# Kernel tuning notes

Hardware: AMD Instinct MI355X
Metric: run time of the kernel (lower is better)

## Reference

```python
import jax, jax.numpy as jnp
import numpy as np

PAD_VALUE = -1e10  # matches torch F.pad(value=-1e10); padded cells are sliced away before output


def setup_inputs() -> dict:
    key = jax.random.key(0)
    x = jax.random.normal(key, (8, 16, 256, 256), dtype=jnp.float32)
    return {"x": x, "d": 5}


def reference(x, d):
    # x: (B, C, H, W). Builds a shift-graph: each pixel connects to the d*d-1
    # pixels in a d x d window; weight = -||f1-f2||^2 * sqrt(di^2+dj^2).
    B, C, H, W = x.shape
    r = d // 2
    id0 = jnp.arange(H * W, dtype=jnp.int32).reshape(H, W)
    img_pad = jnp.pad(x, ((0, 0), (0, 0), (r, r), (r, r)), constant_values=PAD_VALUE)
    ws, edges = [], []
    for i in range(d):
        for j in range(d):
            if i == r and j == r:
                continue
            pos_v = (i - r) * W + (j - r)
            # shifted view of the padded image, aligned with x: (B, C, H, W)
            f1 = img_pad[:, :, i:H + i, j:W + j]
            scale = float(((i - r) ** 2 + (j - r) ** 2) ** 0.5)
            dist = -((f1 - x) ** 2).sum(axis=1) * scale  # (B, H, W)
            # crop to the region where the shifted neighbor is in-bounds
            h0, h1 = max(r - i, 0), H - max(i - r, 0)
            w0, w1 = max(r - j, 0), W - max(j - r, 0)
            imgx = dist[:, h0:h1, w0:w1].reshape(B, -1)  # (B, n_ij)
            idx = id0[h0:h1, w0:w1].reshape(-1)          # (n_ij,)
            pos = jnp.broadcast_to(idx[None, :], (B, idx.shape[0]))
            ws.append(imgx)
            edges.append(jnp.stack((pos, pos + pos_v), axis=-1))  # (B, n_ij, 2)
    return jnp.concatenate(edges, axis=-2), jnp.concatenate(ws, axis=-1)
```

## Files before the change

### kernel.cpp

```cpp
#include <hip/hip_runtime.h>


#define HH 256
#define WW 256
#define CC 16
#define BB 8
#define HW (HH * WW)
#define EE 1557540

__global__ __launch_bounds__(256) void shiftgraph_kernel(
    const float* __restrict__ x, float* __restrict__ out) {
    __shared__ float lds[3080];
    const int bid = blockIdx.x;
    const int b = bid & 7;
    const int h = bid >> 3;
    const int w = threadIdx.x;

    const float* __restrict__ xb = x + (size_t)b * (CC * HW);

    const float* src[3];
    int dst[3];
#pragma unroll
    for (int inst = 0; inst < 3; ++inst) {
        const int flatf = inst * 1024 + w * 4;
        const int cl  = flatf / 768;
        const int rem = flatf - cl * 768;
        const int row = rem >> 8;
        const int col = rem & 255;
        int hr = h + row; hr = hr > HH - 1 ? HH - 1 : hr;
        src[inst] = xb + cl * HW + hr * WW + col;
        dst[inst] = flatf;
    }

    float* __restrict__ edges = out;
    float* __restrict__ wsp   = out + (size_t)BB * EE * 2;
    const size_t bE = (size_t)b * EE;
    const int posc = h * WW + w;

    float acc[12];
#pragma unroll
    for (int s2 = 0; s2 < 12; ++s2) acc[s2] = 0.0f;

#pragma unroll
    for (int cc = 0; cc < 4; ++cc) {
        if (cc > 0) {
            asm volatile("" ::: "memory");
            __builtin_amdgcn_s_barrier();
            __builtin_amdgcn_sched_barrier(0);
        }
#pragma unroll
        for (int inst = 0; inst < 3; ++inst) {
            const float4 v = *reinterpret_cast<const float4*>(src[inst]);
            *reinterpret_cast<float4*>(&lds[dst[inst]]) = v;
            src[inst] += 4 * HW;
        }
        asm volatile("s_waitcnt lgkmcnt(0)" ::: "memory");
        __builtin_amdgcn_s_barrier();
        __builtin_amdgcn_sched_barrier(0);

#pragma unroll
        for (int c = 0; c < 4; ++c) {
            const int base = c * 768 + w;
            const float ctr = lds[base];
            float d;
            d = lds[base + 1] - ctr; acc[0] = fmaf(d, d, acc[0]);
            d = lds[base + 2] - ctr; acc[1] = fmaf(d, d, acc[1]);
#pragma unroll
            for (int dj = -2; dj <= 2; ++dj) {
                d = lds[base + 256 + dj] - ctr;
                acc[4 + dj] = fmaf(d, d, acc[4 + dj]);
                d = lds[base + 512 + dj] - ctr;
                acc[9 + dj] = fmaf(d, d, acc[9 + dj]);
            }
        }

        {
            int s = 0;
#pragma unroll
            for (int di = 0; di <= 2; ++di) {
#pragma unroll
                for (int dj = (di == 0 ? 1 : -2); dj <= 2; ++dj, ++s) {
                    if (s < cc * 3 || s >= cc * 3 + 3) continue;
                    const int i = di + 2, j = dj + 2;
                    if (h + di >= HH) continue;
                    const int w2 = w + dj;
                    if (w2 < 0 || w2 >= WW) continue;

                    int offF = 0, offM = 0;
#pragma unroll
                    for (int m = 0; m < 25; ++m) {
                        const int mi = m / 5, mj = m % 5;
                        if (mi == 2 && mj == 2) continue;
                        const int cm = (HH - (mi < 2 ? 2 - mi : mi - 2)) *
                                       (WW - (mj < 2 ? 2 - mj : mj - 2));
                        if (m < i * 5 + j) offF += cm;
                        if (m < (4 - i) * 5 + (4 - j)) offM += cm;
                    }
                    const int cww = WW - (dj < 0 ? -dj : dj);
                    const int e1 = offF + h * cww + (w - (dj < 0 ? -dj : 0));
                    const int e2 = offM + h * cww + (w + (dj < 0 ? dj : 0));
                    const int posv = di * WW + dj;

                    *reinterpret_cast<float2*>(edges + (bE + e1) * 2) =
                        make_float2((float)posc, (float)(posc + posv));
                    *reinterpret_cast<float2*>(edges + (bE + e2) * 2) =
                        make_float2((float)(posc + posv), (float)posc);
                }
            }
        }
    }

    int s = 0;
#pragma unroll
    for (int di = 0; di <= 2; ++di) {
#pragma unroll
        for (int dj = (di == 0 ? 1 : -2); dj <= 2; ++dj, ++s) {
            const int i = di + 2, j = dj + 2;
            if (h + di >= HH) continue;
            const int w2 = w + dj;
            if (w2 < 0 || w2 >= WW) continue;

            const float scale = sqrtf((float)(di * di + dj * dj));
            const float wsv = -acc[s] * scale;

            int offF = 0, offM = 0;
#pragma unroll
            for (int m = 0; m < 25; ++m) {
                const int mi = m / 5, mj = m % 5;
                if (mi == 2 && mj == 2) continue;
                const int cm = (HH - (mi < 2 ? 2 - mi : mi - 2)) *
                               (WW - (mj < 2 ? 2 - mj : mj - 2));
                if (m < i * 5 + j) offF += cm;
                if (m < (4 - i) * 5 + (4 - j)) offM += cm;
            }
            const int cww = WW - (dj < 0 ? -dj : dj);
            const int e1 = offF + h * cww + (w - (dj < 0 ? -dj : 0));
            const int e2 = offM + h * cww + (w + (dj < 0 ? dj : 0));

            wsp[bE + e1] = wsv;
            wsp[bE + e2] = wsv;
        }
    }
}

extern "C" void kernel_launch(void* const* d_in, const int* in_sizes, int n_in,
                              void* d_out, int out_size, void* d_ws, size_t ws_size,
                              hipStream_t stream) {
    const float* x = (const float*)d_in[0];
    float* out = (float*)d_out;
    dim3 block(WW);
    dim3 grid(HH * BB);
    shiftgraph_kernel<<<grid, block, 0, stream>>>(x, out);
}
```

Before: 32.91 us.

## Transpose LDS tile to channel-interleaved float4 layout for vectorized neighbor reads

Each chunk of 4 channels is now staged in LDS as [row][col][channel], so one float4 LDS read returns all four channels of a neighbour pixel. This replaces 48 scalar LDS reads per chunk with 13 float4 reads. Global loads become 12 scalar loads per thread instead of 3 float4 loads, which costs some global load efficiency. Out-of-range columns are clamped rather than read past the row end.

```diff
diff --git a/kernel.cpp b/kernel.cpp
--- a/kernel.cpp
+++ b/kernel.cpp
@@ -10,7 +10,7 @@
 
 __global__ __launch_bounds__(256) void shiftgraph_kernel(
     const float* __restrict__ x, float* __restrict__ out) {
-    __shared__ float lds[3080];
+    __shared__ float lds[3072];
     const int bid = blockIdx.x;
     const int b = bid & 7;
     const int h = bid >> 3;
@@ -18,19 +18,19 @@
 
     const float* __restrict__ xb = x + (size_t)b * (CC * HW);
 
-    const float* src[3];
-    int dst[3];
+    const int ch = w & 3;
+    const int cq = w >> 2;
+    const float* prow[3];
 #pragma unroll
-    for (int inst = 0; inst < 3; ++inst) {
-        const int flatf = inst * 1024 + w * 4;
-        const int cl  = flatf / 768;
-        const int rem = flatf - cl * 768;
-        const int row = rem >> 8;
-        const int col = rem & 255;
-        int hr = h + row; hr = hr > HH - 1 ? HH - 1 : hr;
-        src[inst] = xb + cl * HW + hr * WW + col;
-        dst[inst] = flatf;
+    for (int r = 0; r < 3; ++r) {
+        int hr = h + r; hr = hr > HH - 1 ? HH - 1 : hr;
+        prow[r] = xb + ch * HW + hr * WW + cq;
     }
+
+    const int wp1 = w + 1 > 255 ? 255 : w + 1;
+    const int wp2 = w + 2 > 255 ? 255 : w + 2;
+    const int wm1 = w - 1 < 0 ? 0 : w - 1;
+    const int wm2 = w - 2 < 0 ? 0 : w - 2;
 
     float* __restrict__ edges = out;
     float* __restrict__ wsp   = out + (size_t)BB * EE * 2;
@@ -41,6 +41,8 @@
 #pragma unroll
     for (int s2 = 0; s2 < 12; ++s2) acc[s2] = 0.0f;
 
+    const float4* __restrict__ ldsv = reinterpret_cast<const float4*>(lds);
+
 #pragma unroll
     for (int cc = 0; cc < 4; ++cc) {
         if (cc > 0) {
@@ -49,29 +51,38 @@
             __builtin_amdgcn_sched_barrier(0);
         }
 #pragma unroll
-        for (int inst = 0; inst < 3; ++inst) {
-            const float4 v = *reinterpret_cast<const float4*>(src[inst]);
-            *reinterpret_cast<float4*>(&lds[dst[inst]]) = v;
-            src[inst] += 4 * HW;
+        for (int inst = 0; inst < 12; ++inst) {
+            const int r = inst >> 2, k = inst & 3;
+            lds[r * 1024 + k * 256 + w] = prow[r][(size_t)cc * 4 * HW + k * 64];
         }
         asm volatile("s_waitcnt lgkmcnt(0)" ::: "memory");
         __builtin_amdgcn_s_barrier();
         __builtin_amdgcn_sched_barrier(0);
 
-#pragma unroll
-        for (int c = 0; c < 4; ++c) {
-            const int base = c * 768 + w;
-            const float ctr = lds[base];
-            float d;
-            d = lds[base + 1] - ctr; acc[0] = fmaf(d, d, acc[0]);
-            d = lds[base + 2] - ctr; acc[1] = fmaf(d, d, acc[1]);
-#pragma unroll
-            for (int dj = -2; dj <= 2; ++dj) {
-                d = lds[base + 256 + dj] - ctr;
-                acc[4 + dj] = fmaf(d, d, acc[4 + dj]);
-                d = lds[base + 512 + dj] - ctr;
-                acc[9 + dj] = fmaf(d, d, acc[9 + dj]);
-            }
+        {
+            const float4 ctr = ldsv[w];
+            float4 nb; float dx, dy, dz, dw_;
+#define ACCUM(IDX, SLOT)                                                   \
+            nb = ldsv[IDX];                                                \
+            dx = nb.x - ctr.x; dy = nb.y - ctr.y;                          \
+            dz = nb.z - ctr.z; dw_ = nb.w - ctr.w;                         \
+            acc[SLOT] = fmaf(dx, dx, acc[SLOT]);                           \
+            acc[SLOT] = fmaf(dy, dy, acc[SLOT]);                           \
+            acc[SLOT] = fmaf(dz, dz, acc[SLOT]);                           \
+            acc[SLOT] = fmaf(dw_, dw_, acc[SLOT]);
+            ACCUM(wp1, 0)
+            ACCUM(wp2, 1)
+            ACCUM(256 + wm2, 2)
+            ACCUM(256 + wm1, 3)
+            ACCUM(256 + w,   4)
+            ACCUM(256 + wp1, 5)
+            ACCUM(256 + wp2, 6)
+            ACCUM(512 + wm2, 7)
+            ACCUM(512 + wm1, 8)
+            ACCUM(512 + w,   9)
+            ACCUM(512 + wp1, 10)
+            ACCUM(512 + wp2, 11)
+#undef ACCUM
         }
 
         {
@@ -110,35 +121,37 @@
         }
     }
 
-    int s = 0;
+    {
+        int s = 0;
 #pragma unroll
-    for (int di = 0; di <= 2; ++di) {
+        for (int di = 0; di <= 2; ++di) {
 #pragma unroll
-        for (int dj = (di == 0 ? 1 : -2); dj <= 2; ++dj, ++s) {
-            const int i = di + 2, j = dj + 2;
-            if (h + di >= HH) continue;
-            const int w2 = w + dj;
-            if (w2 < 0 || w2 >= WW) continue;
+            for (int dj = (di == 0 ? 1 : -2); dj <= 2; ++dj, ++s) {
+                const int i = di + 2, j = dj + 2;
+                if (h + di >= HH) continue;
+                const int w2 = w + dj;
+                if (w2 < 0 || w2 >= WW) continue;
 
-            const float scale = sqrtf((float)(di * di + dj * dj));
-            const float wsv = -acc[s] * scale;
+                const float scale = sqrtf((float)(di * di + dj * dj));
+                const float wsv = -acc[s] * scale;
 
-            int offF = 0, offM = 0;
+                int offF = 0, offM = 0;
 #pragma unroll
-            for (int m = 0; m < 25; ++m) {
-                const int mi = m / 5, mj = m % 5;
-                if (mi == 2 && mj == 2) continue;
-                const int cm = (HH - (mi < 2 ? 2 - mi : mi - 2)) *
-                               (WW - (mj < 2 ? 2 - mj : mj - 2));
-                if (m < i * 5 + j) offF += cm;
-                if (m < (4 - i) * 5 + (4 - j)) offM += cm;
+                for (int m = 0; m < 25; ++m) {
+                    const int mi = m / 5, mj = m % 5;
+                    if (mi == 2 && mj == 2) continue;
+                    const int cm = (HH - (mi < 2 ? 2 - mi : mi - 2)) *
+                                   (WW - (mj < 2 ? 2 - mj : mj - 2));
+                    if (m < i * 5 + j) offF += cm;
+                    if (m < (4 - i) * 5 + (4 - j)) offM += cm;
+                }
+                const int cww = WW - (dj < 0 ? -dj : dj);
+                const int e1 = offF + h * cww + (w - (dj < 0 ? -dj : 0));
+                const int e2 = offM + h * cww + (w + (dj < 0 ? dj : 0));
+
+                wsp[bE + e1] = wsv;
+                wsp[bE + e2] = wsv;
             }
-            const int cww = WW - (dj < 0 ? -dj : dj);
-            const int e1 = offF + h * cww + (w - (dj < 0 ? -dj : 0));
-            const int e2 = offM + h * cww + (w + (dj < 0 ? dj : 0));
-
-            wsp[bE + e1] = wsv;
-            wsp[bE + e2] = wsv;
         }
     }
 }
```

After: 34.65 us. +5.3%, slower.
